# Kernel optimization log

Measured on AMD Instinct MI355X. Metric: run time of the kernel, lower is better.

Reference implementation:

```python
import jax, jax.numpy as jnp
import numpy as np

B, NQ, K = 256, 16, 200           # batch, num_neg+1, num_keys
KEY_SIZE, QUERY_SIZE, HIDDEN = 64, 64, 128
NEG_INF_SCALE = -1000000000.0


def setup_inputs() -> dict:
    key = jax.random.key(0)
    ks = jax.random.split(key, 9)
    queries = jax.random.normal(ks[0], (B, NQ, QUERY_SIZE), dtype=jnp.float32)
    keys = jax.random.normal(ks[1], (B, K, KEY_SIZE), dtype=jnp.float32)
    cum_subs_masks = (jax.random.uniform(ks[2], (B, NQ, K, 1)) < 0.3).astype(jnp.float32)
    s = 1.0 / np.sqrt(HIDDEN)
    Wq = jax.random.normal(ks[3], (QUERY_SIZE, HIDDEN), dtype=jnp.float32) * s
    bq = jnp.zeros((HIDDEN,), dtype=jnp.float32)
    Wk = jax.random.normal(ks[4], (KEY_SIZE, HIDDEN), dtype=jnp.float32) * s
    bk = jnp.zeros((HIDDEN,), dtype=jnp.float32)
    Wv = jax.random.normal(ks[5], (HIDDEN, 1), dtype=jnp.float32) * s
    bv = jnp.zeros((1,), dtype=jnp.float32)
    return {"queries": queries, "keys": keys, "cum_subs_masks": cum_subs_masks,
            "num_neg": NQ - 1, "Wq": Wq, "bq": bq, "Wk": Wk, "bk": bk,
            "Wv": Wv, "bv": bv}


def reference(queries, keys, cum_subs_masks, num_neg, Wq, bq, Wk, bk, Wv, bv):
    # project once, broadcast instead of expanding keys per query (same math)
    qh = queries @ Wq + bq                 # (B, NQ, H)
    kh = keys @ Wk + bk                    # (B, K, H)
    h = jnp.tanh(qh[:, :, None, :] + kh[:, None, :, :])   # (B, NQ, K, H)
    scores = h @ Wv + bv                   # (B, NQ, K, 1)
    if cum_subs_masks is not None:
        scores = scores + cum_subs_masks * NEG_INF_SCALE
    attn_weight = jax.nn.softmax(scores, axis=-2)          # softmax over keys
    attn_out = jnp.sum(attn_weight * keys[:, None, :, :], axis=-2)  # (B, NQ, key_size)
    return (attn_out, attn_weight)
```

## Files before the change

kernel.cpp:

```cpp
#include <hip/hip_runtime.h>
#include <hip/hip_bf16.h>

namespace {

typedef __attribute__((ext_vector_type(8))) short short8;
typedef __attribute__((ext_vector_type(4))) float f32x4;

constexpr int kNB = 256;
constexpr int kNQ = 16;
constexpr int kNK = 200;
constexpr int kDK = 64;
constexpr int kNH = 128;
constexpr int kHK = 100;
constexpr int kS  = 132;
constexpr float kNeg = -1000000000.0f;
constexpr float kC2 = 2.8853900817779268f;

constexpr size_t kWsNeed = (size_t)kNB * kNQ * kNK * sizeof(float);

__device__ __forceinline__ float exp2_hw(float x) {
#if defined(__has_builtin)
# if __has_builtin(__builtin_amdgcn_exp2f)
  return __builtin_amdgcn_exp2f(x);
# else
  return __expf(x * 0.69314718055994531f);
# endif
#else
  return __expf(x * 0.69314718055994531f);
#endif
}

template <int CTRL>
__device__ __forceinline__ float dpp_add(float v) {
  int sw = __builtin_amdgcn_update_dpp(0, __float_as_int(v), CTRL, 0xF, 0xF, true);
  return v + __int_as_float(sw);
}

__device__ __forceinline__ void split8(float4 a, float4 b, short8& hi, short8& lo) {
  float v[8] = {a.x, a.y, a.z, a.w, b.x, b.y, b.z, b.w};
#pragma unroll
  for (int j = 0; j < 8; ++j) {
    const __hip_bfloat16 h = __float2bfloat16(v[j]);
    hi[j] = (short)__bfloat16_as_ushort(h);
    const __hip_bfloat16 l = __float2bfloat16(v[j] - __bfloat162float(h));
    lo[j] = (short)__bfloat16_as_ushort(l);
  }
}

__launch_bounds__(512)
__attribute__((amdgpu_waves_per_eu(4, 4)))
__global__ void proj_score(const float* __restrict__ queries,
                           const float* __restrict__ keys,
                           const float* __restrict__ Wq,
                           const float* __restrict__ bq,
                           const float* __restrict__ Wk,
                           const float* __restrict__ bk,
                           const float* __restrict__ Wv,
                           float* __restrict__ ps) {
  __shared__ float skh[kHK * kS];
  __shared__ float sqh[kNQ * kNH];

  const int tid  = threadIdx.x;
  const int b    = blockIdx.x >> 1;
  const int half = blockIdx.x & 1;
  const int lane = tid & 63;
  const int wave = __builtin_amdgcn_readfirstlane(tid >> 6);
  const int l15  = lane & 15;
  const int q16  = lane >> 4;
  const int hbase = 8 * l15;

  const float* kb = keys + ((size_t)b * kNK + half * kHK) * kDK;
  const float* qb = queries + (size_t)b * kNQ * kDK;

  {
    const int col = wave * 16 + l15;
    const int kj0 = q16 * 8;

    short8 bh[2], bl[2];
#pragma unroll
    for (int p = 0; p < 2; ++p) {
      float4 v0, v1;
      v0.x = Wk[(p * 32 + kj0 + 0) * kNH + col];
      v0.y = Wk[(p * 32 + kj0 + 1) * kNH + col];
      v0.z = Wk[(p * 32 + kj0 + 2) * kNH + col];
      v0.w = Wk[(p * 32 + kj0 + 3) * kNH + col];
      v1.x = Wk[(p * 32 + kj0 + 4) * kNH + col];
      v1.y = Wk[(p * 32 + kj0 + 5) * kNH + col];
      v1.z = Wk[(p * 32 + kj0 + 6) * kNH + col];
      v1.w = Wk[(p * 32 + kj0 + 7) * kNH + col];
      split8(v0, v1, bh[p], bl[p]);
    }
    const float bkc = bk[col];

    for (int tr = 0; tr < 7; ++tr) {
      f32x4 acc = {0.f, 0.f, 0.f, 0.f};
      const int row = tr * 16 + l15;
      const bool ok = row < kHK;
#pragma unroll
      for (int p = 0; p < 2; ++p) {
        float4 a0 = {0.f, 0.f, 0.f, 0.f}, a1 = {0.f, 0.f, 0.f, 0.f};
        if (ok) {
          const float* ap = kb + (size_t)row * kDK + p * 32 + kj0;
          a0 = *reinterpret_cast<const float4*>(ap);
          a1 = *reinterpret_cast<const float4*>(ap + 4);
        }
        short8 ah, al;
        split8(a0, a1, ah, al);
        acc = __builtin_amdgcn_mfma_f32_16x16x32_bf16(al, bh[p], acc, 0, 0, 0);
        acc = __builtin_amdgcn_mfma_f32_16x16x32_bf16(ah, bl[p], acc, 0, 0, 0);
        acc = __builtin_amdgcn_mfma_f32_16x16x32_bf16(ah, bh[p], acc, 0, 0, 0);
      }
#pragma unroll
      for (int r = 0; r < 4; ++r) {
        const int rr = tr * 16 + q16 * 4 + r;
        if (rr < kHK) skh[rr * kS + col] = exp2_hw(kC2 * (acc[r] + bkc));
      }
    }

    {
      short8 qbh[2], qbl[2];
#pragma unroll
      for (int p = 0; p < 2; ++p) {
        float4 v0, v1;
        v0.x = Wq[(p * 32 + kj0 + 0) * kNH + col];
        v0.y = Wq[(p * 32 + kj0 + 1) * kNH + col];
        v0.z = Wq[(p * 32 + kj0 + 2) * kNH + col];
        v0.w = Wq[(p * 32 + kj0 + 3) * kNH + col];
        v1.x = Wq[(p * 32 + kj0 + 4) * kNH + col];
        v1.y = Wq[(p * 32 + kj0 + 5) * kNH + col];
        v1.z = Wq[(p * 32 + kj0 + 6) * kNH + col];
        v1.w = Wq[(p * 32 + kj0 + 7) * kNH + col];
        split8(v0, v1, qbh[p], qbl[p]);
      }
      const float bqc = bq[col];
      f32x4 acc = {0.f, 0.f, 0.f, 0.f};
#pragma unroll
      for (int p = 0; p < 2; ++p) {
        const float* ap = qb + (size_t)l15 * kDK + p * 32 + kj0;
        const float4 a0 = *reinterpret_cast<const float4*>(ap);
        const float4 a1 = *reinterpret_cast<const float4*>(ap + 4);
        short8 ah, al;
        split8(a0, a1, ah, al);
        acc = __builtin_amdgcn_mfma_f32_16x16x32_bf16(al, qbh[p], acc, 0, 0, 0);
        acc = __builtin_amdgcn_mfma_f32_16x16x32_bf16(ah, qbl[p], acc, 0, 0, 0);
        acc = __builtin_amdgcn_mfma_f32_16x16x32_bf16(ah, qbh[p], acc, 0, 0, 0);
      }
#pragma unroll
      for (int r = 0; r < 4; ++r)
        sqh[(q16 * 4 + r) * kNH + col] = exp2_hw(kC2 * (acc[r] + bqc));
    }
  }

  float wv2[8];
  {
    const float4 wva = *reinterpret_cast<const float4*>(&Wv[hbase]);
    const float4 wvb = *reinterpret_cast<const float4*>(&Wv[hbase + 4]);
    wv2[0] = -2.0f * wva.x; wv2[1] = -2.0f * wva.y;
    wv2[2] = -2.0f * wva.z; wv2[3] = -2.0f * wva.w;
    wv2[4] = -2.0f * wvb.x; wv2[5] = -2.0f * wvb.y;
    wv2[6] = -2.0f * wvb.z; wv2[7] = -2.0f * wvb.w;
  }

  __syncthreads();

  const int qg = wave >> 1;
  const int kg = wave & 1;
  float qreg[4][8];
#pragma unroll
  for (int qi = 0; qi < 4; ++qi) {
    const float4 qa  = *reinterpret_cast<const float4*>(&sqh[(4 * qg + qi) * kNH + hbase]);
    const float4 qb4 = *reinterpret_cast<const float4*>(&sqh[(4 * qg + qi) * kNH + hbase + 4]);
    qreg[qi][0] = qa.x;  qreg[qi][1] = qa.y;  qreg[qi][2] = qa.z;  qreg[qi][3] = qa.w;
    qreg[qi][4] = qb4.x; qreg[qi][5] = qb4.y; qreg[qi][6] = qb4.z; qreg[qi][7] = qb4.w;
  }
#pragma unroll
  for (int qi = 0; qi < 4; ++qi)
#pragma unroll
    for (int m = 0; m < 8; ++m) asm volatile("" : "+v"(qreg[qi][m]));

  float* pw = ps + (size_t)b * kNQ * kNK + half * kHK;
  {
    auto score_k = [&](int k) {
      const float* krow = &skh[k * kS + hbase];
      const float4 ka  = *reinterpret_cast<const float4*>(krow);
      const float4 kb4 = *reinterpret_cast<const float4*>(krow + 4);
#pragma unroll
      for (int qi = 0; qi < 4; ++qi) {
        const float e0 = qreg[qi][0] * ka.x;
        const float e1 = qreg[qi][1] * ka.y;
        const float e2 = qreg[qi][2] * ka.z;
        const float e3 = qreg[qi][3] * ka.w;
        const float e4 = qreg[qi][4] * kb4.x;
        const float e5 = qreg[qi][5] * kb4.y;
        const float e6 = qreg[qi][6] * kb4.z;
        const float e7 = qreg[qi][7] * kb4.w;
        const float r0 = __builtin_amdgcn_rcpf(1.0f + e0);
        const float r1 = __builtin_amdgcn_rcpf(1.0f + e1);
        const float r2 = __builtin_amdgcn_rcpf(1.0f + e2);
        const float r3 = __builtin_amdgcn_rcpf(1.0f + e3);
        const float r4 = __builtin_amdgcn_rcpf(1.0f + e4);
        const float r5 = __builtin_amdgcn_rcpf(1.0f + e5);
        const float r6 = __builtin_amdgcn_rcpf(1.0f + e6);
        const float r7 = __builtin_amdgcn_rcpf(1.0f + e7);
        float acc0 = wv2[0] * r0;
        acc0 = fmaf(wv2[1], r1, acc0);
        acc0 = fmaf(wv2[2], r2, acc0);
        acc0 = fmaf(wv2[3], r3, acc0);
        float acc1 = wv2[4] * r4;
        acc1 = fmaf(wv2[5], r5, acc1);
        acc1 = fmaf(wv2[6], r6, acc1);
        acc1 = fmaf(wv2[7], r7, acc1);
        float acc = acc0 + acc1;
        acc = dpp_add<0xB1>(acc);
        acc = dpp_add<0x4E>(acc);
        acc = dpp_add<0x141>(acc);
        acc = dpp_add<0x140>(acc);
        if (l15 == 0) pw[(4 * qg + qi) * kNK + k] = acc;
      }
    };
    for (int i = 0; i < 12; ++i) score_k(8 * i + 4 * kg + q16);
    if (kg == 0) score_k(96 + q16);
  }
}

__launch_bounds__(512)
__global__ void softmax_gemv(const float* __restrict__ keys,
                             const float* __restrict__ masks,
                             const float* __restrict__ ps,
                             float* __restrict__ out_attn,
                             float* __restrict__ out_w) {
  __shared__ float sw[8 * kNK];
  __shared__ float pk[8 * 4 * kDK];

  const int tid  = threadIdx.x;
  const int b    = blockIdx.x >> 1;
  const int qh2  = blockIdx.x & 1;
  const int lane = tid & 63;
  const int wave = __builtin_amdgcn_readfirstlane(tid >> 6);
  const int q    = qh2 * 8 + wave;

  const float* kbase = keys + (size_t)b * kNK * kDK;

  {
    const float* p    = ps    + ((size_t)b * kNQ + q) * kNK;
    const float* mrow = masks + ((size_t)b * kNQ + q) * kNK;
    const bool tail = lane < (kNK - 192);
    float v0 = fmaf(mrow[lane],       kNeg, p[lane]);
    float v1 = fmaf(mrow[lane + 64],  kNeg, p[lane + 64]);
    float v2 = fmaf(mrow[lane + 128], kNeg, p[lane + 128]);
    float v3 = tail ? fmaf(mrow[lane + 192], kNeg, p[lane + 192]) : -1e30f;
    float m = fmaxf(fmaxf(v0, v1), fmaxf(v2, v3));
#pragma unroll
    for (int off = 32; off > 0; off >>= 1) m = fmaxf(m, __shfl_xor(m, off, 64));
    const float e0 = __expf(v0 - m);
    const float e1 = __expf(v1 - m);
    const float e2 = __expf(v2 - m);
    const float e3 = tail ? __expf(v3 - m) : 0.f;
    float sum = (e0 + e1) + (e2 + e3);
#pragma unroll
    for (int off = 32; off > 0; off >>= 1) sum += __shfl_xor(sum, off, 64);
    const float rs = __builtin_amdgcn_rcpf(sum);
    float* og  = out_w + ((size_t)b * kNQ + q) * kNK;
    float* swr = &sw[wave * kNK];
    const float w0 = e0 * rs, w1 = e1 * rs, w2 = e2 * rs, w3 = e3 * rs;
    swr[lane]       = w0;  og[lane]       = w0;
    swr[lane + 64]  = w1;  og[lane + 64]  = w1;
    swr[lane + 128] = w2;  og[lane + 128] = w2;
    if (tail) { swr[lane + 192] = w3; og[lane + 192] = w3; }
  }
  __syncthreads();

  {
    const int qg = wave >> 2;
    const int kg = wave & 3;
    const int kstart = 52 * kg;
    const int kend = (kg == 3) ? kNK : (kstart + 52);
    const float* kb2 = kbase + lane;
    float acc[4] = {0.f, 0.f, 0.f, 0.f};
    for (int k0 = kstart; k0 < kend; k0 += 4) {
      const float kv0 = kb2[(size_t)(k0 + 0) * kDK];
      const float kv1 = kb2[(size_t)(k0 + 1) * kDK];
      const float kv2 = kb2[(size_t)(k0 + 2) * kDK];
      const float kv3 = kb2[(size_t)(k0 + 3) * kDK];
#pragma unroll
      for (int qi = 0; qi < 4; ++qi) {
        const float4 wq = *reinterpret_cast<const float4*>(&sw[(4 * qg + qi) * kNK + k0]);
        acc[qi] = fmaf(wq.x, kv0, acc[qi]);
        acc[qi] = fmaf(wq.y, kv1, acc[qi]);
        acc[qi] = fmaf(wq.z, kv2, acc[qi]);
        acc[qi] = fmaf(wq.w, kv3, acc[qi]);
      }
    }
#pragma unroll
    for (int qi = 0; qi < 4; ++qi)
      pk[((4 * qg + qi) * 4 + kg) * kDK + lane] = acc[qi];
  }
  __syncthreads();

  {
    const float r = pk[(wave * 4 + 0) * kDK + lane] + pk[(wave * 4 + 1) * kDK + lane] +
                    pk[(wave * 4 + 2) * kDK + lane] + pk[(wave * 4 + 3) * kDK + lane];
    out_attn[((size_t)b * kNQ + q) * kDK + lane] = r;
  }
}

constexpr int kThreads = 1024;
constexpr int kKhFloats = kNK * kS;
constexpr int kScFloats = kNQ * kNK;
constexpr int kQhFloats = kNQ * kNH;
constexpr size_t kSmemBytes =
    (size_t)(kKhFloats + kScFloats + kQhFloats) * sizeof(float);

__launch_bounds__(kThreads)
__attribute__((amdgpu_waves_per_eu(4, 4)))
__global__ void bahdanau_fused(const float* __restrict__ queries,
                               const float* __restrict__ keys,
                               const float* __restrict__ masks,
                               const float* __restrict__ Wq,
                               const float* __restrict__ bq,
                               const float* __restrict__ Wk,
                               const float* __restrict__ bk,
                               const float* __restrict__ Wv,
                               float* __restrict__ out_attn,
                               float* __restrict__ out_w) {
  extern __shared__ __align__(16) float smem[];
  float* skh2 = smem;
  float* ssc = smem + kKhFloats;
  float* sqh2 = smem + kKhFloats + kScFloats;

  const int tid  = threadIdx.x;
  const int b    = blockIdx.x;
  const int lane = tid & 63;
  const int wave = __builtin_amdgcn_readfirstlane(tid >> 6);
  const int l15  = lane & 15;
  const int q16  = lane >> 4;
  const int hbase = 8 * l15;

  const float* kb = keys + (size_t)b * kNK * kDK;
  const float* qb = queries + (size_t)b * kNQ * kDK;

  {
    const int tc  = wave >> 1;
    const int odd = wave & 1;
    const int col = tc * 16 + l15;
    const int kj0 = q16 * 8;

    short8 bh[2], bl[2];
#pragma unroll
    for (int p = 0; p < 2; ++p) {
      float4 v0, v1;
      v0.x = Wk[(p * 32 + kj0 + 0) * kNH + col];
      v0.y = Wk[(p * 32 + kj0 + 1) * kNH + col];
      v0.z = Wk[(p * 32 + kj0 + 2) * kNH + col];
      v0.w = Wk[(p * 32 + kj0 + 3) * kNH + col];
      v1.x = Wk[(p * 32 + kj0 + 4) * kNH + col];
      v1.y = Wk[(p * 32 + kj0 + 5) * kNH + col];
      v1.z = Wk[(p * 32 + kj0 + 6) * kNH + col];
      v1.w = Wk[(p * 32 + kj0 + 7) * kNH + col];
      split8(v0, v1, bh[p], bl[p]);
    }
    const float bkc = bk[col];
    const int trB = odd ? 7 : 0;
    const int trE = odd ? 13 : 7;
    for (int tr = trB; tr < trE; ++tr) {
      f32x4 acc = {0.f, 0.f, 0.f, 0.f};
      const int row = tr * 16 + l15;
      const bool ok = row < kNK;
#pragma unroll
      for (int p = 0; p < 2; ++p) {
        float4 a0 = {0.f, 0.f, 0.f, 0.f}, a1 = {0.f, 0.f, 0.f, 0.f};
        if (ok) {
          const float* ap = kb + (size_t)row * kDK + p * 32 + kj0;
          a0 = *reinterpret_cast<const float4*>(ap);
          a1 = *reinterpret_cast<const float4*>(ap + 4);
        }
        short8 ah, al;
        split8(a0, a1, ah, al);
        acc = __builtin_amdgcn_mfma_f32_16x16x32_bf16(al, bh[p], acc, 0, 0, 0);
        acc = __builtin_amdgcn_mfma_f32_16x16x32_bf16(ah, bl[p], acc, 0, 0, 0);
        acc = __builtin_amdgcn_mfma_f32_16x16x32_bf16(ah, bh[p], acc, 0, 0, 0);
      }
#pragma unroll
      for (int r = 0; r < 4; ++r) {
        const int rr = tr * 16 + q16 * 4 + r;
        if (rr < kNK) skh2[(size_t)rr * kS + col] = exp2_hw(kC2 * (acc[r] + bkc));
      }
    }
    if (odd) {
      short8 qbh[2], qbl[2];
#pragma unroll
      for (int p = 0; p < 2; ++p) {
        float4 v0, v1;
        v0.x = Wq[(p * 32 + kj0 + 0) * kNH + col];
        v0.y = Wq[(p * 32 + kj0 + 1) * kNH + col];
        v0.z = Wq[(p * 32 + kj0 + 2) * kNH + col];
        v0.w = Wq[(p * 32 + kj0 + 3) * kNH + col];
        v1.x = Wq[(p * 32 + kj0 + 4) * kNH + col];
        v1.y = Wq[(p * 32 + kj0 + 5) * kNH + col];
        v1.z = Wq[(p * 32 + kj0 + 6) * kNH + col];
        v1.w = Wq[(p * 32 + kj0 + 7) * kNH + col];
        split8(v0, v1, qbh[p], qbl[p]);
      }
      const float bqc = bq[col];
      f32x4 acc = {0.f, 0.f, 0.f, 0.f};
#pragma unroll
      for (int p = 0; p < 2; ++p) {
        const float* ap = qb + (size_t)l15 * kDK + p * 32 + kj0;
        const float4 a0 = *reinterpret_cast<const float4*>(ap);
        const float4 a1 = *reinterpret_cast<const float4*>(ap + 4);
        short8 ah, al;
        split8(a0, a1, ah, al);
        acc = __builtin_amdgcn_mfma_f32_16x16x32_bf16(al, qbh[p], acc, 0, 0, 0);
        acc = __builtin_amdgcn_mfma_f32_16x16x32_bf16(ah, qbl[p], acc, 0, 0, 0);
        acc = __builtin_amdgcn_mfma_f32_16x16x32_bf16(ah, qbh[p], acc, 0, 0, 0);
      }
#pragma unroll
      for (int r = 0; r < 4; ++r)
        sqh2[(size_t)(q16 * 4 + r) * kNH + col] = exp2_hw(kC2 * (acc[r] + bqc));
    }
  }

  float wv2[8];
  {
    const float4 wva = *reinterpret_cast<const float4*>(&Wv[hbase]);
    const float4 wvb = *reinterpret_cast<const float4*>(&Wv[hbase + 4]);
    wv2[0] = -2.0f * wva.x; wv2[1] = -2.0f * wva.y;
    wv2[2] = -2.0f * wva.z; wv2[3] = -2.0f * wva.w;
    wv2[4] = -2.0f * wvb.x; wv2[5] = -2.0f * wvb.y;
    wv2[6] = -2.0f * wvb.z; wv2[7] = -2.0f * wvb.w;
  }

  __syncthreads();

  const int qg = wave >> 2;
  const int kg = wave & 3;
  float qreg[4][8];
#pragma unroll
  for (int qi = 0; qi < 4; ++qi) {
    const float4 qa  = *reinterpret_cast<const float4*>(&sqh2[(4 * qg + qi) * kNH + hbase]);
    const float4 qb4 = *reinterpret_cast<const float4*>(&sqh2[(4 * qg + qi) * kNH + hbase + 4]);
    qreg[qi][0] = qa.x;  qreg[qi][1] = qa.y;  qreg[qi][2] = qa.z;  qreg[qi][3] = qa.w;
    qreg[qi][4] = qb4.x; qreg[qi][5] = qb4.y; qreg[qi][6] = qb4.z; qreg[qi][7] = qb4.w;
  }

  {
    auto score_k = [&](int k) {
      const float* krow = &skh2[(size_t)k * kS + hbase];
      const float4 ka  = *reinterpret_cast<const float4*>(krow);
      const float4 kb4 = *reinterpret_cast<const float4*>(krow + 4);
#pragma unroll
      for (int qi = 0; qi < 4; ++qi) {
        const float e0 = qreg[qi][0] * ka.x;
        const float e1 = qreg[qi][1] * ka.y;
        const float e2 = qreg[qi][2] * ka.z;
        const float e3 = qreg[qi][3] * ka.w;
        const float e4 = qreg[qi][4] * kb4.x;
        const float e5 = qreg[qi][5] * kb4.y;
        const float e6 = qreg[qi][6] * kb4.z;
        const float e7 = qreg[qi][7] * kb4.w;
        const float r0 = __builtin_amdgcn_rcpf(1.0f + e0);
        const float r1 = __builtin_amdgcn_rcpf(1.0f + e1);
        const float r2 = __builtin_amdgcn_rcpf(1.0f + e2);
        const float r3 = __builtin_amdgcn_rcpf(1.0f + e3);
        const float r4 = __builtin_amdgcn_rcpf(1.0f + e4);
        const float r5 = __builtin_amdgcn_rcpf(1.0f + e5);
        const float r6 = __builtin_amdgcn_rcpf(1.0f + e6);
        const float r7 = __builtin_amdgcn_rcpf(1.0f + e7);
        float acc0 = wv2[0] * r0;
        acc0 = fmaf(wv2[1], r1, acc0);
        acc0 = fmaf(wv2[2], r2, acc0);
        acc0 = fmaf(wv2[3], r3, acc0);
        float acc1 = wv2[4] * r4;
        acc1 = fmaf(wv2[5], r5, acc1);
        acc1 = fmaf(wv2[6], r6, acc1);
        acc1 = fmaf(wv2[7], r7, acc1);
        float acc = acc0 + acc1;
        acc = dpp_add<0xB1>(acc);
        acc = dpp_add<0x4E>(acc);
        acc = dpp_add<0x141>(acc);
        acc = dpp_add<0x140>(acc);
        if (l15 == 0) ssc[(4 * qg + qi) * kNK + k] = acc;
      }
    };
    for (int i = 0; i < 12; ++i) score_k(16 * i + 4 * kg + q16);
    if (kg < 2) score_k(192 + 4 * kg + q16);
  }

  const float* mrow = masks + ((size_t)b * kNQ + wave) * kNK;
  const bool tail = lane < (kNK - 192);
  const float mm0 = mrow[lane];
  const float mm1 = mrow[lane + 64];
  const float mm2 = mrow[lane + 128];
  const float mm3 = tail ? mrow[lane + 192] : 0.0f;

  __syncthreads();

  {
    const float* sr = &ssc[wave * kNK];
    float v0 = fmaf(mm0, kNeg, sr[lane]);
    float v1 = fmaf(mm1, kNeg, sr[lane + 64]);
    float v2 = fmaf(mm2, kNeg, sr[lane + 128]);
    float v3 = tail ? fmaf(mm3, kNeg, sr[lane + 192]) : -1e30f;
    float m = fmaxf(fmaxf(v0, v1), fmaxf(v2, v3));
#pragma unroll
    for (int off = 32; off > 0; off >>= 1) m = fmaxf(m, __shfl_xor(m, off, 64));
    const float e0 = __expf(v0 - m);
    const float e1 = __expf(v1 - m);
    const float e2 = __expf(v2 - m);
    const float e3 = tail ? __expf(v3 - m) : 0.f;
    float sum = (e0 + e1) + (e2 + e3);
#pragma unroll
    for (int off = 32; off > 0; off >>= 1) sum += __shfl_xor(sum, off, 64);
    const float rs = __builtin_amdgcn_rcpf(sum);
    float* og = out_w + ((size_t)b * kNQ + wave) * kNK;
    float* swr = &ssc[wave * kNK];
    const float w0 = e0 * rs, w1 = e1 * rs, w2 = e2 * rs, w3 = e3 * rs;
    swr[lane]       = w0;  og[lane]       = w0;
    swr[lane + 64]  = w1;  og[lane + 64]  = w1;
    swr[lane + 128] = w2;  og[lane + 128] = w2;
    if (tail) { swr[lane + 192] = w3; og[lane + 192] = w3; }
  }
  __syncthreads();

  {
    float* pk2 = skh2;
    const int kstart = 52 * kg;
    const int kend = (kg == 3) ? kNK : (kstart + 52);
    const float* kb2 = kb + lane;
    float acc[4] = {0.f, 0.f, 0.f, 0.f};
    for (int k0 = kstart; k0 < kend; k0 += 4) {
      const float kv0 = kb2[(size_t)(k0 + 0) * kDK];
      const float kv1 = kb2[(size_t)(k0 + 1) * kDK];
      const float kv2 = kb2[(size_t)(k0 + 2) * kDK];
      const float kv3 = kb2[(size_t)(k0 + 3) * kDK];
#pragma unroll
      for (int qi = 0; qi < 4; ++qi) {
        const float4 wq = *reinterpret_cast<const float4*>(&ssc[(4 * qg + qi) * kNK + k0]);
        acc[qi] = fmaf(wq.x, kv0, acc[qi]);
        acc[qi] = fmaf(wq.y, kv1, acc[qi]);
        acc[qi] = fmaf(wq.z, kv2, acc[qi]);
        acc[qi] = fmaf(wq.w, kv3, acc[qi]);
      }
    }
#pragma unroll
    for (int qi = 0; qi < 4; ++qi)
      pk2[((4 * qg + qi) * 4 + kg) * kDK + lane] = acc[qi];
  }
  __syncthreads();

  {
    const float* pk2 = skh2;
    const float r = pk2[(wave * 4 + 0) * kDK + lane] + pk2[(wave * 4 + 1) * kDK + lane] +
                    pk2[(wave * 4 + 2) * kDK + lane] + pk2[(wave * 4 + 3) * kDK + lane];
    out_attn[((size_t)b * kNQ + wave) * kDK + lane] = r;
  }
}

}

extern "C" void kernel_launch(void* const* d_in, const int* in_sizes, int n_in,
                              void* d_out, int out_size, void* d_ws, size_t ws_size,
                              hipStream_t stream) {
  const float* queries = (const float*)d_in[0];
  const float* keys    = (const float*)d_in[1];
  const float* masks   = (const float*)d_in[2];
  const float* Wq = (const float*)d_in[4];
  const float* bq = (const float*)d_in[5];
  const float* Wk = (const float*)d_in[6];
  const float* bk = (const float*)d_in[7];
  const float* Wv = (const float*)d_in[8];

  float* out_attn = (float*)d_out;
  float* out_w    = out_attn + (size_t)kNB * kNQ * kDK;

  if (ws_size >= kWsNeed) {
    float* ps = (float*)d_ws;
    proj_score<<<kNB * 2, 512, 0, stream>>>(queries, keys, Wq, bq, Wk, bk, Wv, ps);
    softmax_gemv<<<kNB * 2, 512, 0, stream>>>(keys, masks, ps, out_attn, out_w);
  } else {
    hipFuncSetAttribute((const void*)bahdanau_fused,
                        hipFuncAttributeMaxDynamicSharedMemorySize, (int)kSmemBytes);
    bahdanau_fused<<<kNB, kThreads, kSmemBytes, stream>>>(queries, keys, masks, Wq, bq,
                                                          Wk, bk, Wv, out_attn, out_w);
  }
}
```

Baseline: 42.82 us.

## Split proj_score into quarter-key blocks with higher occupancy target

The projection/score kernel now splits each batch row's keys into four 50-key chunks instead of two 100-key halves, launching four times the batch count of blocks. Each wave handles 2 queries across all keys in its chunk rather than 4 queries over a half of the keys, and the occupancy hint rises from 4 to 8 waves per EU. The aim is more parallelism and better latency hiding in the tanh-score stage. The cost is that the query projection and the Wk/Wq loads are repeated in twice as many blocks, and the score loop has some wasted padded iterations.

```diff
diff --git a/kernel.cpp b/kernel.cpp
--- a/kernel.cpp
+++ b/kernel.cpp
@@ -11,7 +11,7 @@
 constexpr int kNK = 200;
 constexpr int kDK = 64;
 constexpr int kNH = 128;
-constexpr int kHK = 100;
+constexpr int kQK = 50;
 constexpr int kS  = 132;
 constexpr float kNeg = -1000000000.0f;
 constexpr float kC2 = 2.8853900817779268f;
@@ -48,7 +48,7 @@
 }
 
 __launch_bounds__(512)
-__attribute__((amdgpu_waves_per_eu(4, 4)))
+__attribute__((amdgpu_waves_per_eu(8, 8)))
 __global__ void proj_score(const float* __restrict__ queries,
                            const float* __restrict__ keys,
                            const float* __restrict__ Wq,
@@ -57,19 +57,19 @@
                            const float* __restrict__ bk,
                            const float* __restrict__ Wv,
                            float* __restrict__ ps) {
-  __shared__ float skh[kHK * kS];
+  __shared__ float skh[kQK * kS];
   __shared__ float sqh[kNQ * kNH];
 
   const int tid  = threadIdx.x;
-  const int b    = blockIdx.x >> 1;
-  const int half = blockIdx.x & 1;
+  const int b    = blockIdx.x >> 2;
+  const int kq   = blockIdx.x & 3;
   const int lane = tid & 63;
   const int wave = __builtin_amdgcn_readfirstlane(tid >> 6);
   const int l15  = lane & 15;
   const int q16  = lane >> 4;
   const int hbase = 8 * l15;
 
-  const float* kb = keys + ((size_t)b * kNK + half * kHK) * kDK;
+  const float* kb = keys + ((size_t)b * kNK + kq * kQK) * kDK;
   const float* qb = queries + (size_t)b * kNQ * kDK;
 
   {
@@ -92,10 +92,11 @@
     }
     const float bkc = bk[col];
 
-    for (int tr = 0; tr < 7; ++tr) {
+#pragma unroll
+    for (int tr = 0; tr < 4; ++tr) {
       f32x4 acc = {0.f, 0.f, 0.f, 0.f};
       const int row = tr * 16 + l15;
-      const bool ok = row < kHK;
+      const bool ok = row < kQK;
 #pragma unroll
       for (int p = 0; p < 2; ++p) {
         float4 a0 = {0.f, 0.f, 0.f, 0.f}, a1 = {0.f, 0.f, 0.f, 0.f};
@@ -113,7 +114,7 @@
 #pragma unroll
       for (int r = 0; r < 4; ++r) {
         const int rr = tr * 16 + q16 * 4 + r;
-        if (rr < kHK) skh[rr * kS + col] = exp2_hw(kC2 * (acc[r] + bkc));
+        if (rr < kQK) skh[rr * kS + col] = exp2_hw(kC2 * (acc[r] + bkc));
       }
     }
 
@@ -163,63 +164,60 @@
 
   __syncthreads();
 
-  const int qg = wave >> 1;
-  const int kg = wave & 1;
-  float qreg[4][8];
-#pragma unroll
-  for (int qi = 0; qi < 4; ++qi) {
-    const float4 qa  = *reinterpret_cast<const float4*>(&sqh[(4 * qg + qi) * kNH + hbase]);
-    const float4 qb4 = *reinterpret_cast<const float4*>(&sqh[(4 * qg + qi) * kNH + hbase + 4]);
+  float qreg[2][8];
+#pragma unroll
+  for (int qi = 0; qi < 2; ++qi) {
+    const int q = 2 * wave + qi;
+    const float4 qa  = *reinterpret_cast<const float4*>(&sqh[q * kNH + hbase]);
+    const float4 qb4 = *reinterpret_cast<const float4*>(&sqh[q * kNH + hbase + 4]);
     qreg[qi][0] = qa.x;  qreg[qi][1] = qa.y;  qreg[qi][2] = qa.z;  qreg[qi][3] = qa.w;
     qreg[qi][4] = qb4.x; qreg[qi][5] = qb4.y; qreg[qi][6] = qb4.z; qreg[qi][7] = qb4.w;
   }
 #pragma unroll
-  for (int qi = 0; qi < 4; ++qi)
+  for (int qi = 0; qi < 2; ++qi)
 #pragma unroll
     for (int m = 0; m < 8; ++m) asm volatile("" : "+v"(qreg[qi][m]));
 
-  float* pw = ps + (size_t)b * kNQ * kNK + half * kHK;
-  {
-    auto score_k = [&](int k) {
-      const float* krow = &skh[k * kS + hbase];
-      const float4 ka  = *reinterpret_cast<const float4*>(krow);
-      const float4 kb4 = *reinterpret_cast<const float4*>(krow + 4);
-#pragma unroll
-      for (int qi = 0; qi < 4; ++qi) {
-        const float e0 = qreg[qi][0] * ka.x;
-        const float e1 = qreg[qi][1] * ka.y;
-        const float e2 = qreg[qi][2] * ka.z;
-        const float e3 = qreg[qi][3] * ka.w;
-        const float e4 = qreg[qi][4] * kb4.x;
-        const float e5 = qreg[qi][5] * kb4.y;
-        const float e6 = qreg[qi][6] * kb4.z;
-        const float e7 = qreg[qi][7] * kb4.w;
-        const float r0 = __builtin_amdgcn_rcpf(1.0f + e0);
-        const float r1 = __builtin_amdgcn_rcpf(1.0f + e1);
-        const float r2 = __builtin_amdgcn_rcpf(1.0f + e2);
-        const float r3 = __builtin_amdgcn_rcpf(1.0f + e3);
-        const float r4 = __builtin_amdgcn_rcpf(1.0f + e4);
-        const float r5 = __builtin_amdgcn_rcpf(1.0f + e5);
-        const float r6 = __builtin_amdgcn_rcpf(1.0f + e6);
-        const float r7 = __builtin_amdgcn_rcpf(1.0f + e7);
-        float acc0 = wv2[0] * r0;
-        acc0 = fmaf(wv2[1], r1, acc0);
-        acc0 = fmaf(wv2[2], r2, acc0);
-        acc0 = fmaf(wv2[3], r3, acc0);
-        float acc1 = wv2[4] * r4;
-        acc1 = fmaf(wv2[5], r5, acc1);
-        acc1 = fmaf(wv2[6], r6, acc1);
-        acc1 = fmaf(wv2[7], r7, acc1);
-        float acc = acc0 + acc1;
-        acc = dpp_add<0xB1>(acc);
-        acc = dpp_add<0x4E>(acc);
-        acc = dpp_add<0x141>(acc);
-        acc = dpp_add<0x140>(acc);
-        if (l15 == 0) pw[(4 * qg + qi) * kNK + k] = acc;
-      }
-    };
-    for (int i = 0; i < 12; ++i) score_k(8 * i + 4 * kg + q16);
-    if (kg == 0) score_k(96 + q16);
+  float* pw = ps + (size_t)b * kNQ * kNK + kq * kQK;
+  for (int i = 0; i < 13; ++i) {
+    const int k = 4 * i + q16;
+    const int kr = (k < kQK) ? k : (kQK - 1);
+    const float* krow = &skh[kr * kS + hbase];
+    const float4 ka  = *reinterpret_cast<const float4*>(krow);
+    const float4 kb4 = *reinterpret_cast<const float4*>(krow + 4);
+#pragma unroll
+    for (int qi = 0; qi < 2; ++qi) {
+      const float e0 = qreg[qi][0] * ka.x;
+      const float e1 = qreg[qi][1] * ka.y;
+      const float e2 = qreg[qi][2] * ka.z;
+      const float e3 = qreg[qi][3] * ka.w;
+      const float e4 = qreg[qi][4] * kb4.x;
+      const float e5 = qreg[qi][5] * kb4.y;
+      const float e6 = qreg[qi][6] * kb4.z;
+      const float e7 = qreg[qi][7] * kb4.w;
+      const float r0 = __builtin_amdgcn_rcpf(1.0f + e0);
+      const float r1 = __builtin_amdgcn_rcpf(1.0f + e1);
+      const float r2 = __builtin_amdgcn_rcpf(1.0f + e2);
+      const float r3 = __builtin_amdgcn_rcpf(1.0f + e3);
+      const float r4 = __builtin_amdgcn_rcpf(1.0f + e4);
+      const float r5 = __builtin_amdgcn_rcpf(1.0f + e5);
+      const float r6 = __builtin_amdgcn_rcpf(1.0f + e6);
+      const float r7 = __builtin_amdgcn_rcpf(1.0f + e7);
+      float acc0 = wv2[0] * r0;
+      acc0 = fmaf(wv2[1], r1, acc0);
+      acc0 = fmaf(wv2[2], r2, acc0);
+      acc0 = fmaf(wv2[3], r3, acc0);
+      float acc1 = wv2[4] * r4;
+      acc1 = fmaf(wv2[5], r5, acc1);
+      acc1 = fmaf(wv2[6], r6, acc1);
+      acc1 = fmaf(wv2[7], r7, acc1);
+      float acc = acc0 + acc1;
+      acc = dpp_add<0xB1>(acc);
+      acc = dpp_add<0x4E>(acc);
+      acc = dpp_add<0x141>(acc);
+      acc = dpp_add<0x140>(acc);
+      if (l15 == 0 && k < kQK) pw[(2 * wave + qi) * kNK + k] = acc;
+    }
   }
 }
 
@@ -575,7 +573,7 @@
 
   if (ws_size >= kWsNeed) {
     float* ps = (float*)d_ws;
-    proj_score<<<kNB * 2, 512, 0, stream>>>(queries, keys, Wq, bq, Wk, bk, Wv, ps);
+    proj_score<<<kNB * 4, 512, 0, stream>>>(queries, keys, Wq, bq, Wk, bk, Wv, ps);
     softmax_gemv<<<kNB * 2, 512, 0, stream>>>(keys, masks, ps, out_attn, out_w);
   } else {
     hipFuncSetAttribute((const void*)bahdanau_fused,
```

After: 46.15 us. 1.08x slower.

## Fuse projection-score and softmax-gemv kernels into one per-batch kernel

Applied to the files above, without the earlier changes.

Replaces the two-kernel workspace path (proj_score with 512 blocks, then softmax_gemv with 512 blocks) with a single 1024-thread kernel per batch row. Each block computes the full key projection, scores, softmax and weighted sum, using the global workspace only for score exchange within the block. This removes a kernel launch and the split of key rows across two blocks. The cost is half as many blocks (256) and larger shared memory per block, which may reduce occupancy. The tanh denominators also switch from a separate multiply plus add to a single fma.

```diff
diff --git a/kernel.cpp b/kernel.cpp
--- a/kernel.cpp
+++ b/kernel.cpp
@@ -11,10 +11,16 @@
 constexpr int kNK = 200;
 constexpr int kDK = 64;
 constexpr int kNH = 128;
-constexpr int kHK = 100;
-constexpr int kS  = 132;
+constexpr int kThreads = 1024;
+constexpr int kS = 132;
 constexpr float kNeg = -1000000000.0f;
 constexpr float kC2 = 2.8853900817779268f;
+
+constexpr int kKhFloats = kNK * kS;
+constexpr int kScFloats = kNQ * kNK;
+constexpr int kQhFloats = kNQ * kNH;
+constexpr size_t kSmemBytes =
+    (size_t)(kKhFloats + kScFloats + kQhFloats) * sizeof(float);
 
 constexpr size_t kWsNeed = (size_t)kNB * kNQ * kNK * sizeof(float);
 
@@ -47,33 +53,39 @@
   }
 }
 
-__launch_bounds__(512)
+__launch_bounds__(kThreads)
 __attribute__((amdgpu_waves_per_eu(4, 4)))
-__global__ void proj_score(const float* __restrict__ queries,
-                           const float* __restrict__ keys,
-                           const float* __restrict__ Wq,
-                           const float* __restrict__ bq,
-                           const float* __restrict__ Wk,
-                           const float* __restrict__ bk,
-                           const float* __restrict__ Wv,
-                           float* __restrict__ ps) {
-  __shared__ float skh[kHK * kS];
-  __shared__ float sqh[kNQ * kNH];
+__global__ void bahdanau_fused_ws(const float* __restrict__ queries,
+                                  const float* __restrict__ keys,
+                                  const float* __restrict__ masks,
+                                  const float* __restrict__ Wq,
+                                  const float* __restrict__ bq,
+                                  const float* __restrict__ Wk,
+                                  const float* __restrict__ bk,
+                                  const float* __restrict__ Wv,
+                                  float* __restrict__ ps,
+                                  float* __restrict__ out_attn,
+                                  float* __restrict__ out_w) {
+  extern __shared__ __align__(16) float smem[];
+  float* skh = smem;
+  float* ssc = smem + kKhFloats;
+  float* sqh = smem + kKhFloats + kScFloats;
 
   const int tid  = threadIdx.x;
-  const int b    = blockIdx.x >> 1;
-  const int half = blockIdx.x & 1;
+  const int b    = blockIdx.x;
   const int lane = tid & 63;
   const int wave = __builtin_amdgcn_readfirstlane(tid >> 6);
   const int l15  = lane & 15;
   const int q16  = lane >> 4;
   const int hbase = 8 * l15;
 
-  const float* kb = keys + ((size_t)b * kNK + half * kHK) * kDK;
+  const float* kb = keys + (size_t)b * kNK * kDK;
   const float* qb = queries + (size_t)b * kNQ * kDK;
 
   {
-    const int col = wave * 16 + l15;
+    const int tc  = wave >> 1;
+    const int odd = wave & 1;
+    const int col = tc * 16 + l15;
     const int kj0 = q16 * 8;
 
     short8 bh[2], bl[2];
@@ -92,10 +104,12 @@
     }
     const float bkc = bk[col];
 
-    for (int tr = 0; tr < 7; ++tr) {
+    const int trB = odd ? 7 : 0;
+    const int trE = odd ? 13 : 7;
+    for (int tr = trB; tr < trE; ++tr) {
       f32x4 acc = {0.f, 0.f, 0.f, 0.f};
       const int row = tr * 16 + l15;
-      const bool ok = row < kHK;
+      const bool ok = row < kNK;
 #pragma unroll
       for (int p = 0; p < 2; ++p) {
         float4 a0 = {0.f, 0.f, 0.f, 0.f}, a1 = {0.f, 0.f, 0.f, 0.f};
@@ -113,11 +127,11 @@
 #pragma unroll
       for (int r = 0; r < 4; ++r) {
         const int rr = tr * 16 + q16 * 4 + r;
-        if (rr < kHK) skh[rr * kS + col] = exp2_hw(kC2 * (acc[r] + bkc));
-      }
-    }
-
-    {
+        if (rr < kNK) skh[(size_t)rr * kS + col] = exp2_hw(kC2 * (acc[r] + bkc));
+      }
+    }
+
+    if (odd) {
       short8 qbh[2], qbl[2];
 #pragma unroll
       for (int p = 0; p < 2; ++p) {
@@ -147,7 +161,7 @@
       }
 #pragma unroll
       for (int r = 0; r < 4; ++r)
-        sqh[(q16 * 4 + r) * kNH + col] = exp2_hw(kC2 * (acc[r] + bqc));
+        sqh[(size_t)(q16 * 4 + r) * kNH + col] = exp2_hw(kC2 * (acc[r] + bqc));
     }
   }
 
@@ -163,8 +177,8 @@
 
   __syncthreads();
 
-  const int qg = wave >> 1;
-  const int kg = wave & 1;
+  const int qg = wave >> 2;
+  const int kg = wave & 3;
   float qreg[4][8];
 #pragma unroll
   for (int qi = 0; qi < 4; ++qi) {
@@ -178,30 +192,22 @@
 #pragma unroll
     for (int m = 0; m < 8; ++m) asm volatile("" : "+v"(qreg[qi][m]));
 
-  float* pw = ps + (size_t)b * kNQ * kNK + half * kHK;
+  float* pw = ps + (size_t)b * kNQ * kNK;
   {
     auto score_k = [&](int k) {
-      const float* krow = &skh[k * kS + hbase];
+      const float* krow = &skh[(size_t)k * kS + hbase];
       const float4 ka  = *reinterpret_cast<const float4*>(krow);
       const float4 kb4 = *reinterpret_cast<const float4*>(krow + 4);
 #pragma unroll
       for (int qi = 0; qi < 4; ++qi) {
-        const float e0 = qreg[qi][0] * ka.x;
-        const float e1 = qreg[qi][1] * ka.y;
-        const float e2 = qreg[qi][2] * ka.z;
-        const float e3 = qreg[qi][3] * ka.w;
-        const float e4 = qreg[qi][4] * kb4.x;
-        const float e5 = qreg[qi][5] * kb4.y;
-        const float e6 = qreg[qi][6] * kb4.z;
-        const float e7 = qreg[qi][7] * kb4.w;
-        const float r0 = __builtin_amdgcn_rcpf(1.0f + e0);
-        const float r1 = __builtin_amdgcn_rcpf(1.0f + e1);
-        const float r2 = __builtin_amdgcn_rcpf(1.0f + e2);
-        const float r3 = __builtin_amdgcn_rcpf(1.0f + e3);
-        const float r4 = __builtin_amdgcn_rcpf(1.0f + e4);
-        const float r5 = __builtin_amdgcn_rcpf(1.0f + e5);
-        const float r6 = __builtin_amdgcn_rcpf(1.0f + e6);
-        const float r7 = __builtin_amdgcn_rcpf(1.0f + e7);
+        const float r0 = __builtin_amdgcn_rcpf(fmaf(qreg[qi][0], ka.x, 1.0f));
+        const float r1 = __builtin_amdgcn_rcpf(fmaf(qreg[qi][1], ka.y, 1.0f));
+        const float r2 = __builtin_amdgcn_rcpf(fmaf(qreg[qi][2], ka.z, 1.0f));
+        const float r3 = __builtin_amdgcn_rcpf(fmaf(qreg[qi][3], ka.w, 1.0f));
+        const float r4 = __builtin_amdgcn_rcpf(fmaf(qreg[qi][4], kb4.x, 1.0f));
+        const float r5 = __builtin_amdgcn_rcpf(fmaf(qreg[qi][5], kb4.y, 1.0f));
+        const float r6 = __builtin_amdgcn_rcpf(fmaf(qreg[qi][6], kb4.z, 1.0f));
+        const float r7 = __builtin_amdgcn_rcpf(fmaf(qreg[qi][7], kb4.w, 1.0f));
         float acc0 = wv2[0] * r0;
         acc0 = fmaf(wv2[1], r1, acc0);
         acc0 = fmaf(wv2[2], r2, acc0);
@@ -218,37 +224,26 @@
         if (l15 == 0) pw[(4 * qg + qi) * kNK + k] = acc;
       }
     };
-    for (int i = 0; i < 12; ++i) score_k(8 * i + 4 * kg + q16);
-    if (kg == 0) score_k(96 + q16);
-  }
-}
-
-__launch_bounds__(512)
-__global__ void softmax_gemv(const float* __restrict__ keys,
-                             const float* __restrict__ masks,
-                             const float* __restrict__ ps,
-                             float* __restrict__ out_attn,
-                             float* __restrict__ out_w) {
-  __shared__ float sw[8 * kNK];
-  __shared__ float pk[8 * 4 * kDK];
-
-  const int tid  = threadIdx.x;
-  const int b    = blockIdx.x >> 1;
-  const int qh2  = blockIdx.x & 1;
-  const int lane = tid & 63;
-  const int wave = __builtin_amdgcn_readfirstlane(tid >> 6);
-  const int q    = qh2 * 8 + wave;
-
-  const float* kbase = keys + (size_t)b * kNK * kDK;
-
-  {
-    const float* p    = ps    + ((size_t)b * kNQ + q) * kNK;
-    const float* mrow = masks + ((size_t)b * kNQ + q) * kNK;
-    const bool tail = lane < (kNK - 192);
-    float v0 = fmaf(mrow[lane],       kNeg, p[lane]);
-    float v1 = fmaf(mrow[lane + 64],  kNeg, p[lane + 64]);
-    float v2 = fmaf(mrow[lane + 128], kNeg, p[lane + 128]);
-    float v3 = tail ? fmaf(mrow[lane + 192], kNeg, p[lane + 192]) : -1e30f;
+#pragma unroll
+    for (int i = 0; i < 12; ++i) score_k(16 * i + 4 * kg + q16);
+    if (kg < 2) score_k(192 + 4 * kg + q16);
+  }
+
+  const float* mrow = masks + ((size_t)b * kNQ + wave) * kNK;
+  const bool tail = lane < (kNK - 192);
+  const float mm0 = mrow[lane];
+  const float mm1 = mrow[lane + 64];
+  const float mm2 = mrow[lane + 128];
+  const float mm3 = tail ? mrow[lane + 192] : 0.0f;
+
+  __syncthreads();
+
+  {
+    const float* sr = pw + (size_t)wave * kNK;
+    float v0 = fmaf(mm0, kNeg, sr[lane]);
+    float v1 = fmaf(mm1, kNeg, sr[lane + 64]);
+    float v2 = fmaf(mm2, kNeg, sr[lane + 128]);
+    float v3 = tail ? fmaf(mm3, kNeg, sr[lane + 192]) : -1e30f;
     float m = fmaxf(fmaxf(v0, v1), fmaxf(v2, v3));
 #pragma unroll
     for (int off = 32; off > 0; off >>= 1) m = fmaxf(m, __shfl_xor(m, off, 64));
@@ -260,8 +255,8 @@
 #pragma unroll
     for (int off = 32; off > 0; off >>= 1) sum += __shfl_xor(sum, off, 64);
     const float rs = __builtin_amdgcn_rcpf(sum);
-    float* og  = out_w + ((size_t)b * kNQ + q) * kNK;
-    float* swr = &sw[wave * kNK];
+    float* og = out_w + ((size_t)b * kNQ + wave) * kNK;
+    float* swr = &ssc[wave * kNK];
     const float w0 = e0 * rs, w1 = e1 * rs, w2 = e2 * rs, w3 = e3 * rs;
     swr[lane]       = w0;  og[lane]       = w0;
     swr[lane + 64]  = w1;  og[lane + 64]  = w1;
@@ -271,11 +266,10 @@
   __syncthreads();
 
   {
-    const int qg = wave >> 2;
-    const int kg = wave & 3;
+    float* pk = skh;
     const int kstart = 52 * kg;
     const int kend = (kg == 3) ? kNK : (kstart + 52);
-    const float* kb2 = kbase + lane;
+    const float* kb2 = kb + lane;
     float acc[4] = {0.f, 0.f, 0.f, 0.f};
     for (int k0 = kstart; k0 < kend; k0 += 4) {
       const float kv0 = kb2[(size_t)(k0 + 0) * kDK];
@@ -284,7 +278,7 @@
       const float kv3 = kb2[(size_t)(k0 + 3) * kDK];
 #pragma unroll
       for (int qi = 0; qi < 4; ++qi) {
-        const float4 wq = *reinterpret_cast<const float4*>(&sw[(4 * qg + qi) * kNK + k0]);
+        const float4 wq = *reinterpret_cast<const float4*>(&ssc[(4 * qg + qi) * kNK + k0]);
         acc[qi] = fmaf(wq.x, kv0, acc[qi]);
         acc[qi] = fmaf(wq.y, kv1, acc[qi]);
         acc[qi] = fmaf(wq.z, kv2, acc[qi]);
@@ -298,18 +292,12 @@
   __syncthreads();
 
   {
+    const float* pk = skh;
     const float r = pk[(wave * 4 + 0) * kDK + lane] + pk[(wave * 4 + 1) * kDK + lane] +
                     pk[(wave * 4 + 2) * kDK + lane] + pk[(wave * 4 + 3) * kDK + lane];
-    out_attn[((size_t)b * kNQ + q) * kDK + lane] = r;
-  }
-}
-
-constexpr int kThreads = 1024;
-constexpr int kKhFloats = kNK * kS;
-constexpr int kScFloats = kNQ * kNK;
-constexpr int kQhFloats = kNQ * kNH;
-constexpr size_t kSmemBytes =
-    (size_t)(kKhFloats + kScFloats + kQhFloats) * sizeof(float);
+    out_attn[((size_t)b * kNQ + wave) * kDK + lane] = r;
+  }
+}
 
 __launch_bounds__(kThreads)
 __attribute__((amdgpu_waves_per_eu(4, 4)))
@@ -324,9 +312,9 @@
                                float* __restrict__ out_attn,
                                float* __restrict__ out_w) {
   extern __shared__ __align__(16) float smem[];
-  float* skh2 = smem;
+  float* skh = smem;
   float* ssc = smem + kKhFloats;
-  float* sqh2 = smem + kKhFloats + kScFloats;
+  float* sqh = smem + kKhFloats + kScFloats;
 
   const int tid  = threadIdx.x;
   const int b    = blockIdx.x;
@@ -383,7 +371,7 @@
 #pragma unroll
       for (int r = 0; r < 4; ++r) {
         const int rr = tr * 16 + q16 * 4 + r;
-        if (rr < kNK) skh2[(size_t)rr * kS + col] = exp2_hw(kC2 * (acc[r] + bkc));
+        if (rr < kNK) skh[(size_t)rr * kS + col] = exp2_hw(kC2 * (acc[r] + bkc));
       }
     }
     if (odd) {
@@ -416,7 +404,7 @@
       }
 #pragma unroll
       for (int r = 0; r < 4; ++r)
-        sqh2[(size_t)(q16 * 4 + r) * kNH + col] = exp2_hw(kC2 * (acc[r] + bqc));
+        sqh[(size_t)(q16 * 4 + r) * kNH + col] = exp2_hw(kC2 * (acc[r] + bqc));
     }
   }
 
@@ -437,35 +425,27 @@
   float qreg[4][8];
 #pragma unroll
   for (int qi = 0; qi < 4; ++qi) {
-    const float4 qa  = *reinterpret_cast<const float4*>(&sqh2[(4 * qg + qi) * kNH + hbase]);
-    const float4 qb4 = *reinterpret_cast<const float4*>(&sqh2[(4 * qg + qi) * kNH + hbase + 4]);
+    const float4 qa  = *reinterpret_cast<const float4*>(&sqh[(4 * qg + qi) * kNH + hbase]);
+    const float4 qb4 = *reinterpret_cast<const float4*>(&sqh[(4 * qg + qi) * kNH + hbase + 4]);
     qreg[qi][0] = qa.x;  qreg[qi][1] = qa.y;  qreg[qi][2] = qa.z;  qreg[qi][3] = qa.w;
     qreg[qi][4] = qb4.x; qreg[qi][5] = qb4.y; qreg[qi][6] = qb4.z; qreg[qi][7] = qb4.w;
   }
 
   {
     auto score_k = [&](int k) {
-      const float* krow = &skh2[(size_t)k * kS + hbase];
+      const float* krow = &skh[(size_t)k * kS + hbase];
       const float4 ka  = *reinterpret_cast<const float4*>(krow);
       const float4 kb4 = *reinterpret_cast<const float4*>(krow + 4);
 #pragma unroll
       for (int qi = 0; qi < 4; ++qi) {
-        const float e0 = qreg[qi][0] * ka.x;
-        const float e1 = qreg[qi][1] * ka.y;
-        const float e2 = qreg[qi][2] * ka.z;
-        const float e3 = qreg[qi][3] * ka.w;
-        const float e4 = qreg[qi][4] * kb4.x;
-        const float e5 = qreg[qi][5] * kb4.y;
-        const float e6 = qreg[qi][6] * kb4.z;
-        const float e7 = qreg[qi][7] * kb4.w;
-        const float r0 = __builtin_amdgcn_rcpf(1.0f + e0);
-        const float r1 = __builtin_amdgcn_rcpf(1.0f + e1);
-        const float r2 = __builtin_amdgcn_rcpf(1.0f + e2);
-        const float r3 = __builtin_amdgcn_rcpf(1.0f + e3);
-        const float r4 = __builtin_amdgcn_rcpf(1.0f + e4);
-        const float r5 = __builtin_amdgcn_rcpf(1.0f + e5);
-        const float r6 = __builtin_amdgcn_rcpf(1.0f + e6);
-        const float r7 = __builtin_amdgcn_rcpf(1.0f + e7);
+        const float r0 = __builtin_amdgcn_rcpf(fmaf(qreg[qi][0], ka.x, 1.0f));
+        const float r1 = __builtin_amdgcn_rcpf(fmaf(qreg[qi][1], ka.y, 1.0f));
+        const float r2 = __builtin_amdgcn_rcpf(fmaf(qreg[qi][2], ka.z, 1.0f));
+        const float r3 = __builtin_amdgcn_rcpf(fmaf(qreg[qi][3], ka.w, 1.0f));
+        const float r4 = __builtin_amdgcn_rcpf(fmaf(qreg[qi][4], kb4.x, 1.0f));
+        const float r5 = __builtin_amdgcn_rcpf(fmaf(qreg[qi][5], kb4.y, 1.0f));
+        const float r6 = __builtin_amdgcn_rcpf(fmaf(qreg[qi][6], kb4.z, 1.0f));
+        const float r7 = __builtin_amdgcn_rcpf(fmaf(qreg[qi][7], kb4.w, 1.0f));
         float acc0 = wv2[0] * r0;
         acc0 = fmaf(wv2[1], r1, acc0);
         acc0 = fmaf(wv2[2], r2, acc0);
@@ -523,7 +503,7 @@
   __syncthreads();
 
   {
-    float* pk2 = skh2;
+    float* pk = skh;
     const int kstart = 52 * kg;
     const int kend = (kg == 3) ? kNK : (kstart + 52);
     const float* kb2 = kb + lane;
@@ -544,14 +524,14 @@
     }
 #pragma unroll
     for (int qi = 0; qi < 4; ++qi)
-      pk2[((4 * qg + qi) * 4 + kg) * kDK + lane] = acc[qi];
-  }
-  __syncthreads();
-
-  {
-    const float* pk2 = skh2;
-    const float r = pk2[(wave * 4 + 0) * kDK + lane] + pk2[(wave * 4 + 1) * kDK + lane] +
-                    pk2[(wave * 4 + 2) * kDK + lane] + pk2[(wave * 4 + 3) * kDK + lane];
+      pk[((4 * qg + qi) * 4 + kg) * kDK + lane] = acc[qi];
+  }
+  __syncthreads();
+
+  {
+    const float* pk = skh;
+    const float r = pk[(wave * 4 + 0) * kDK + lane] + pk[(wave * 4 + 1) * kDK + lane] +
+                    pk[(wave * 4 + 2) * kDK + lane] + pk[(wave * 4 + 3) * kDK + lane];
     out_attn[((size_t)b * kNQ + wave) * kDK + lane] = r;
   }
 }
@@ -575,8 +555,10 @@
 
   if (ws_size >= kWsNeed) {
     float* ps = (float*)d_ws;
-    proj_score<<<kNB * 2, 512, 0, stream>>>(queries, keys, Wq, bq, Wk, bk, Wv, ps);
-    softmax_gemv<<<kNB * 2, 512, 0, stream>>>(keys, masks, ps, out_attn, out_w);
+    hipFuncSetAttribute((const void*)bahdanau_fused_ws,
+                        hipFuncAttributeMaxDynamicSharedMemorySize, (int)kSmemBytes);
+    bahdanau_fused_ws<<<kNB, kThreads, kSmemBytes, stream>>>(
+        queries, keys, masks, Wq, bq, Wk, bk, Wv, ps, out_attn, out_w);
   } else {
     hipFuncSetAttribute((const void*)bahdanau_fused,
                         hipFuncAttributeMaxDynamicSharedMemorySize, (int)kSmemBytes);
```

Result: faster. 39.49 us (-7.8%).
